# Kernel tuning notes

Measured on AMD Instinct MI355X. Metric: run time of the kernel, lower is better.

The kernel has to match this reference:

```python
import jax, jax.numpy as jnp
import numpy as np

TEMPERATURE = 8.0  # sqrt(dim_k=64)
NEG_INF = -1e30    # stand-in for -inf that stays finite-safe under softmax


def setup_inputs() -> dict:
    key = jax.random.key(0)
    kq, kk, kv, km = jax.random.split(key, 4)
    bsz, lq, lk, d = 64, 2048, 2048, 64
    q = jax.random.normal(kq, (bsz, lq, d), dtype=jnp.float32)
    k = jax.random.normal(kk, (bsz, lk, d), dtype=jnp.float32)
    v = jax.random.normal(kv, (bsz, lk, d), dtype=jnp.float32)
    mask = jax.random.normal(km, (bsz, lq, lk), dtype=jnp.float32)
    return {"q": q, "k": k, "v": v, "mask": mask}


def reference(q, k, v, mask):
    # attn = QK^T / temperature, additive graph mask, threshold -inf fill
    attn = jnp.einsum("bqd,bkd->bqk", q, k) / TEMPERATURE
    attn = attn + mask                       # graph_mask_type == 'add'
    attn = jnp.where(mask < 0, NEG_INF, attn)  # masked_fill(mask.lt(0), -inf)
    attn = jax.nn.softmax(attn, axis=2)
    # dropout p=0.0 -> identity
    output = jnp.einsum("bqk,bkd->bqd", attn, v)
    return (output, attn)
```

## Files before the change

kernel.cpp:

```cpp
#include <hip/hip_runtime.h>
#include <stdint.h>
#include <stddef.h>


typedef __attribute__((ext_vector_type(4))) float f32x4;
typedef __fp16 f16x2 __attribute__((ext_vector_type(2)));
typedef __fp16 f16x4 __attribute__((ext_vector_type(4)));
typedef __fp16 f16x8 __attribute__((ext_vector_type(8)));

static constexpr int BATCH = 64;
static constexpr int SEQ   = 2048;
static constexpr int HD    = 64;
static constexpr float NEGH = -60000.0f;


__global__ void cvt_f16_kernel(const float* __restrict__ in,
                               __fp16* __restrict__ out, int n4) {
  int i = blockIdx.x * blockDim.x + threadIdx.x;
  if (i >= n4) return;
  f32x4 v = *(const f32x4*)(in + (size_t)i * 4);
  f16x4 o;
  o[0] = (__fp16)v[0]; o[1] = (__fp16)v[1];
  o[2] = (__fp16)v[2]; o[3] = (__fp16)v[3];
  *(f16x4*)(out + (size_t)i * 4) = o;
}

__global__ __launch_bounds__(256, 2) void attn_kernel(
    const __fp16* __restrict__ qh,
    const __fp16* __restrict__ kh,
    const __fp16* __restrict__ vh,
    const float* __restrict__ mask,
    float* __restrict__ out,
    float* __restrict__ attn) {
  __shared__ __align__(16) char pool[4][11520];
  __shared__ float stat_m[4][16];
  __shared__ float stat_l[4][16];

  const int tid  = threadIdx.x;
  const int w    = tid >> 6;
  const int lane = tid & 63;
  const int l15  = lane & 15;
  const int g    = lane >> 4;
  const int g4   = g << 2;
  const int g8   = g << 3;
  const int krow = lane >> 3;
  const int kc16 = (lane & 7) * 16;

  const int bid = blockIdx.x;
  const int xcd = bid & 7;
  const int r   = bid >> 3;
  const int b   = xcd * 8 + (r >> 7);
  const int q0  = (r & 127) << 4;
  const int wk0 = w << 9;

  char* wb = pool[w];

  const __fp16* qptr = qh + ((size_t)(b * SEQ + q0 + l15)) * HD;
  const f16x8 qb0 = *(const f16x8*)(qptr + g8);
  const f16x8 qb1 = *(const f16x8*)(qptr + 32 + g8);

  const __fp16* kstrip = kh + ((size_t)(b * SEQ) + wk0) * HD;
  const __fp16* vstrip = vh + ((size_t)(b * SEQ) + wk0) * HD;
  const float*  mbase  = mask + ((size_t)(b * SEQ + q0)) * SEQ + wk0;
  float*        abase  = attn + ((size_t)(b * SEQ + q0)) * SEQ + wk0;

  f16x4 PH0,  PH1,  PH2,  PH3,  PH4,  PH5,  PH6,  PH7;
  f16x4 PH8,  PH9,  PH10, PH11, PH12, PH13, PH14, PH15;
  f16x4 PH16, PH17, PH18, PH19, PH20, PH21, PH22, PH23;
  f16x4 PH24, PH25, PH26, PH27, PH28, PH29, PH30, PH31;

  f16x8 K0A, K0B, K1A, K1B, K2A, K2B, K3A, K3B;
  f16x8 K4A, K4B, K5A, K5B, K6A, K6B, K7A, K7B;
  f32x4 MA0, MA1, MA2, MA3;
  f32x4 MB0, MB1, MB2, MB3;
  float m = -3.0e38f;

#define ISSUE_K(t, KA, KB)                                                   \
  KA = *(const f16x8*)(kstrip + (size_t)(t) * 1024 + lane * 8);              \
  KB = *(const f16x8*)(kstrip + (size_t)(t) * 1024 + 512 + lane * 8);

#define WRITE_K(s, KA, KB)                                                   \
  *(f16x8*)(wb + (s) * 2304 + krow * 144 + kc16) = KA;                       \
  *(f16x8*)(wb + (s) * 2304 + (8 + krow) * 144 + kc16) = KB;

#define ISSUE_M(c, M0, M1, M2, M3)                                           \
  M0 = __builtin_nontemporal_load((const f32x4*)(mbase + (size_t)(0 * 4 + g) * SEQ + (c) * 64 + l15 * 4)); \
  M1 = __builtin_nontemporal_load((const f32x4*)(mbase + (size_t)(1 * 4 + g) * SEQ + (c) * 64 + l15 * 4)); \
  M2 = __builtin_nontemporal_load((const f32x4*)(mbase + (size_t)(2 * 4 + g) * SEQ + (c) * 64 + l15 * 4)); \
  M3 = __builtin_nontemporal_load((const f32x4*)(mbase + (size_t)(3 * 4 + g) * SEQ + (c) * 64 + l15 * 4));

#define WRITE_M(M0, M1, M2, M3)                                              \
  *(f32x4*)(wb + 7168 + (0 * 4 + g) * 272 + l15 * 16) = M0;                  \
  *(f32x4*)(wb + 7168 + (1 * 4 + g) * 272 + l15 * 16) = M1;                  \
  *(f32x4*)(wb + 7168 + (2 * 4 + g) * 272 + l15 * 16) = M2;                  \
  *(f32x4*)(wb + 7168 + (3 * 4 + g) * 272 + l15 * 16) = M3;

#define ATILE(t, s, PH)                                                      \
  {                                                                          \
    const f16x8 fa = *(const f16x8*)(wb + (s) * 2304 + l15 * 144 + g * 16);  \
    const f16x8 fb = *(const f16x8*)(wb + (s) * 2304 + l15 * 144 + 64 + g * 16); \
    f32x4 acc = {0.f, 0.f, 0.f, 0.f};                                        \
    acc = __builtin_amdgcn_mfma_f32_16x16x32_f16(fa, qb0, acc, 0, 0, 0);     \
    acc = __builtin_amdgcn_mfma_f32_16x16x32_f16(fb, qb1, acc, 0, 0, 0);     \
    const f32x4 mv = *(const f32x4*)(wb + 7168 + l15 * 272 + ((t) & 3) * 64 + g * 16); \
    float s0 = (mv[0] < 0.f) ? NEGH : fmaf(acc[0], 0.125f, mv[0]);           \
    float s1 = (mv[1] < 0.f) ? NEGH : fmaf(acc[1], 0.125f, mv[1]);           \
    float s2 = (mv[2] < 0.f) ? NEGH : fmaf(acc[2], 0.125f, mv[2]);           \
    float s3 = (mv[3] < 0.f) ? NEGH : fmaf(acc[3], 0.125f, mv[3]);           \
    m = fmaxf(m, fmaxf(fmaxf(s0, s1), fmaxf(s2, s3)));                       \
    f16x2 lo_ = __builtin_amdgcn_cvt_pkrtz(s0, s1);                          \
    f16x2 hi_ = __builtin_amdgcn_cvt_pkrtz(s2, s3);                          \
    PH = (f16x4){lo_[0], lo_[1], hi_[0], hi_[1]};                            \
  }

#define AT(t, PH, KA, KB)                                                    \
  WRITE_K((t) & 1, KA, KB) ISSUE_K((t) + 8, KA, KB) ATILE(t, (t) & 1, PH)
#define ATL(t, PH, KA, KB)                                                   \
  WRITE_K((t) & 1, KA, KB) ATILE(t, (t) & 1, PH)

  ISSUE_M(0, MA0, MA1, MA2, MA3)
  ISSUE_K(0, K0A, K0B) ISSUE_K(1, K1A, K1B) ISSUE_K(2, K2A, K2B) ISSUE_K(3, K3A, K3B)
  ISSUE_M(1, MB0, MB1, MB2, MB3)
  ISSUE_K(4, K4A, K4B) ISSUE_K(5, K5A, K5B) ISSUE_K(6, K6A, K6B) ISSUE_K(7, K7A, K7B)

  WRITE_M(MA0, MA1, MA2, MA3) ISSUE_M(2, MA0, MA1, MA2, MA3)
  AT(0, PH0, K0A, K0B)  AT(1, PH1, K1A, K1B)  AT(2, PH2, K2A, K2B)  AT(3, PH3, K3A, K3B)
  WRITE_M(MB0, MB1, MB2, MB3) ISSUE_M(3, MB0, MB1, MB2, MB3)
  AT(4, PH4, K4A, K4B)  AT(5, PH5, K5A, K5B)  AT(6, PH6, K6A, K6B)  AT(7, PH7, K7A, K7B)
  WRITE_M(MA0, MA1, MA2, MA3) ISSUE_M(4, MA0, MA1, MA2, MA3)
  AT(8, PH8, K0A, K0B)  AT(9, PH9, K1A, K1B)  AT(10, PH10, K2A, K2B) AT(11, PH11, K3A, K3B)
  WRITE_M(MB0, MB1, MB2, MB3) ISSUE_M(5, MB0, MB1, MB2, MB3)
  AT(12, PH12, K4A, K4B) AT(13, PH13, K5A, K5B) AT(14, PH14, K6A, K6B) AT(15, PH15, K7A, K7B)
  WRITE_M(MA0, MA1, MA2, MA3) ISSUE_M(6, MA0, MA1, MA2, MA3)
  AT(16, PH16, K0A, K0B) AT(17, PH17, K1A, K1B) AT(18, PH18, K2A, K2B) AT(19, PH19, K3A, K3B)
  WRITE_M(MB0, MB1, MB2, MB3) ISSUE_M(7, MB0, MB1, MB2, MB3)
  AT(20, PH20, K4A, K4B) AT(21, PH21, K5A, K5B) AT(22, PH22, K6A, K6B) AT(23, PH23, K7A, K7B)
  WRITE_M(MA0, MA1, MA2, MA3)
  ATL(24, PH24, K0A, K0B) ATL(25, PH25, K1A, K1B) ATL(26, PH26, K2A, K2B) ATL(27, PH27, K3A, K3B)
  WRITE_M(MB0, MB1, MB2, MB3)
  ATL(28, PH28, K4A, K4B) ATL(29, PH29, K5A, K5B) ATL(30, PH30, K6A, K6B) ATL(31, PH31, K7A, K7B)

#undef AT
#undef ATL
#undef ATILE
#undef ISSUE_K
#undef WRITE_K
#undef ISSUE_M
#undef WRITE_M

  m = fmaxf(m, __shfl_xor(m, 16));
  m = fmaxf(m, __shfl_xor(m, 32));

  float lw = 0.f;
#define A2_STEP(PH)                                                          \
  {                                                                          \
    float e0 = __expf((float)PH[0] - m);                                     \
    float e1 = __expf((float)PH[1] - m);                                     \
    float e2 = __expf((float)PH[2] - m);                                     \
    float e3 = __expf((float)PH[3] - m);                                     \
    lw += (e0 + e1) + (e2 + e3);                                             \
    f16x2 lo_ = __builtin_amdgcn_cvt_pkrtz(e0, e1);                          \
    f16x2 hi_ = __builtin_amdgcn_cvt_pkrtz(e2, e3);                          \
    PH = (f16x4){lo_[0], lo_[1], hi_[0], hi_[1]};                            \
  }
  A2_STEP(PH0)  A2_STEP(PH1)  A2_STEP(PH2)  A2_STEP(PH3)
  A2_STEP(PH4)  A2_STEP(PH5)  A2_STEP(PH6)  A2_STEP(PH7)
  A2_STEP(PH8)  A2_STEP(PH9)  A2_STEP(PH10) A2_STEP(PH11)
  A2_STEP(PH12) A2_STEP(PH13) A2_STEP(PH14) A2_STEP(PH15)
  A2_STEP(PH16) A2_STEP(PH17) A2_STEP(PH18) A2_STEP(PH19)
  A2_STEP(PH20) A2_STEP(PH21) A2_STEP(PH22) A2_STEP(PH23)
  A2_STEP(PH24) A2_STEP(PH25) A2_STEP(PH26) A2_STEP(PH27)
  A2_STEP(PH28) A2_STEP(PH29) A2_STEP(PH30) A2_STEP(PH31)
#undef A2_STEP

  lw += __shfl_xor(lw, 16);
  lw += __shfl_xor(lw, 32);

  if (lane < 16) { stat_m[w][lane] = m; stat_l[w][lane] = lw; }
  __syncthreads();

  float mg = -3.0e38f;
#pragma unroll
  for (int ww = 0; ww < 4; ++ww) mg = fmaxf(mg, stat_m[ww][l15]);
  float lg = 0.f;
#pragma unroll
  for (int ww = 0; ww < 4; ++ww) lg += stat_l[ww][l15] * __expf(stat_m[ww][l15] - mg);
  const float scale = __expf(m - mg) / lg;
  const __fp16 hs = (__fp16)scale;
  const f16x4 sc4 = {hs, hs, hs, hs};

  f32x4 oacc0 = {0.f, 0.f, 0.f, 0.f};
  f32x4 oacc1 = {0.f, 0.f, 0.f, 0.f};
  f32x4 oacc2 = {0.f, 0.f, 0.f, 0.f};
  f32x4 oacc3 = {0.f, 0.f, 0.f, 0.f};

  f16x8 V0A, V0B, V1A, V1B, V2A, V2B, V3A, V3B;

#define ISSUE_V(t, VA, VB)                                                   \
  VA = *(const f16x8*)(vstrip + (size_t)(t) * 1024 + lane * 8);              \
  VB = *(const f16x8*)(vstrip + (size_t)(t) * 1024 + 512 + lane * 8);

#define WRITE_VT(VA, VB)                                                     \
  {                                                                          \
    char* p_ = wb + 4608 + ((lane & 7) * 8) * 40 + krow * 2;                 \
    *(__fp16*)(p_ + 0 * 40) = VA[0]; *(__fp16*)(p_ + 1 * 40) = VA[1];        \
    *(__fp16*)(p_ + 2 * 40) = VA[2]; *(__fp16*)(p_ + 3 * 40) = VA[3];        \
    *(__fp16*)(p_ + 4 * 40) = VA[4]; *(__fp16*)(p_ + 5 * 40) = VA[5];        \
    *(__fp16*)(p_ + 6 * 40) = VA[6]; *(__fp16*)(p_ + 7 * 40) = VA[7];        \
    char* q_ = p_ + 16;                                                      \
    *(__fp16*)(q_ + 0 * 40) = VB[0]; *(__fp16*)(q_ + 1 * 40) = VB[1];        \
    *(__fp16*)(q_ + 2 * 40) = VB[2]; *(__fp16*)(q_ + 3 * 40) = VB[3];        \
    *(__fp16*)(q_ + 4 * 40) = VB[4]; *(__fp16*)(q_ + 5 * 40) = VB[5];        \
    *(__fp16*)(q_ + 6 * 40) = VB[6]; *(__fp16*)(q_ + 7 * 40) = VB[7];        \
  }

#define BTILE(t, PH)                                                         \
  {                                                                          \
    const f16x4 pf = PH * sc4;                                               \
    f32x4 st;                                                                \
    st[0] = (float)pf[0]; st[1] = (float)pf[1];                              \
    st[2] = (float)pf[2]; st[3] = (float)pf[3];                              \
    *(f32x4*)(wb + 7168 + l15 * 272 + ((t) & 3) * 64 + g * 16) = st;         \
    const char* vf_ = wb + 4608 + l15 * 40 + g * 8;                          \
    const f16x4 Vr0_ = *(const f16x4*)(vf_ + 0 * 640);                       \
    const f16x4 Vr1_ = *(const f16x4*)(vf_ + 1 * 640);                       \
    const f16x4 Vr2_ = *(const f16x4*)(vf_ + 2 * 640);                       \
    const f16x4 Vr3_ = *(const f16x4*)(vf_ + 3 * 640);                       \
    oacc0 = __builtin_amdgcn_mfma_f32_16x16x16f16(Vr0_, pf, oacc0, 0, 0, 0); \
    oacc1 = __builtin_amdgcn_mfma_f32_16x16x16f16(Vr1_, pf, oacc1, 0, 0, 0); \
    oacc2 = __builtin_amdgcn_mfma_f32_16x16x16f16(Vr2_, pf, oacc2, 0, 0, 0); \
    oacc3 = __builtin_amdgcn_mfma_f32_16x16x16f16(Vr3_, pf, oacc3, 0, 0, 0); \
  }

#define STORE_A(c)                                                           \
  __builtin_nontemporal_store(                                               \
      *(const f32x4*)(wb + 7168 + (0 * 4 + g) * 272 + l15 * 16),             \
      (f32x4*)(abase + (size_t)(0 * 4 + g) * SEQ + (c) * 64 + l15 * 4));     \
  __builtin_nontemporal_store(                                               \
      *(const f32x4*)(wb + 7168 + (1 * 4 + g) * 272 + l15 * 16),             \
      (f32x4*)(abase + (size_t)(1 * 4 + g) * SEQ + (c) * 64 + l15 * 4));     \
  __builtin_nontemporal_store(                                               \
      *(const f32x4*)(wb + 7168 + (2 * 4 + g) * 272 + l15 * 16),             \
      (f32x4*)(abase + (size_t)(2 * 4 + g) * SEQ + (c) * 64 + l15 * 4));     \
  __builtin_nontemporal_store(                                               \
      *(const f32x4*)(wb + 7168 + (3 * 4 + g) * 272 + l15 * 16),             \
      (f32x4*)(abase + (size_t)(3 * 4 + g) * SEQ + (c) * 64 + l15 * 4));

#define BSTEP(t, PH, VA, VB)   BTILE(t, PH) WRITE_VT(VA, VB) ISSUE_V((t) + 5, VA, VB)
#define BSTEPN(t, PH, VA, VB)  BTILE(t, PH) WRITE_VT(VA, VB)
#define BSTEPL(t, PH)          BTILE(t, PH)

  ISSUE_V(0, V0A, V0B) ISSUE_V(1, V1A, V1B) ISSUE_V(2, V2A, V2B) ISSUE_V(3, V3A, V3B)
  WRITE_VT(V0A, V0B)
  ISSUE_V(4, V0A, V0B)

  BSTEP(0, PH0, V1A, V1B)   BSTEP(1, PH1, V2A, V2B)   BSTEP(2, PH2, V3A, V3B)
  BSTEP(3, PH3, V0A, V0B)   STORE_A(0)
  BSTEP(4, PH4, V1A, V1B)   BSTEP(5, PH5, V2A, V2B)   BSTEP(6, PH6, V3A, V3B)
  BSTEP(7, PH7, V0A, V0B)   STORE_A(1)
  BSTEP(8, PH8, V1A, V1B)   BSTEP(9, PH9, V2A, V2B)   BSTEP(10, PH10, V3A, V3B)
  BSTEP(11, PH11, V0A, V0B) STORE_A(2)
  BSTEP(12, PH12, V1A, V1B) BSTEP(13, PH13, V2A, V2B) BSTEP(14, PH14, V3A, V3B)
  BSTEP(15, PH15, V0A, V0B) STORE_A(3)
  BSTEP(16, PH16, V1A, V1B) BSTEP(17, PH17, V2A, V2B) BSTEP(18, PH18, V3A, V3B)
  BSTEP(19, PH19, V0A, V0B) STORE_A(4)
  BSTEP(20, PH20, V1A, V1B) BSTEP(21, PH21, V2A, V2B) BSTEP(22, PH22, V3A, V3B)
  BSTEP(23, PH23, V0A, V0B) STORE_A(5)
  BSTEP(24, PH24, V1A, V1B) BSTEP(25, PH25, V2A, V2B) BSTEP(26, PH26, V3A, V3B)
  BSTEPN(27, PH27, V0A, V0B) STORE_A(6)
  BSTEPN(28, PH28, V1A, V1B) BSTEPN(29, PH29, V2A, V2B) BSTEPN(30, PH30, V3A, V3B)
  BSTEPL(31, PH31)           STORE_A(7)

#undef BSTEP
#undef BSTEPN
#undef BSTEPL
#undef BTILE
#undef WRITE_VT
#undef ISSUE_V
#undef STORE_A

  float* sred_w = (float*)pool[w];
#pragma unroll
  for (int rr = 0; rr < 4; ++rr) {
    sred_w[(0 * 16 + g4 + rr) * 17 + l15] = oacc0[rr];
    sred_w[(1 * 16 + g4 + rr) * 17 + l15] = oacc1[rr];
    sred_w[(2 * 16 + g4 + rr) * 17 + l15] = oacc2[rr];
    sred_w[(3 * 16 + g4 + rr) * 17 + l15] = oacc3[rr];
  }
  __syncthreads();

#pragma unroll
  for (int ii = 0; ii < 4; ++ii) {
    const int i = tid + ii * 256;
    const int q = i >> 6;
    const int d = i & 63;
    const int o = d * 17 + q;
    float s = ((const float*)pool[0])[o] + ((const float*)pool[1])[o] +
              ((const float*)pool[2])[o] + ((const float*)pool[3])[o];
    out[((size_t)(b * SEQ + q0 + q)) * HD + d] = s;
  }
}

extern "C" void kernel_launch(void* const* d_in, const int* in_sizes, int n_in,
                              void* d_out, int out_size, void* d_ws, size_t ws_size,
                              hipStream_t stream) {
  const float* q    = (const float*)d_in[0];
  const float* k    = (const float*)d_in[1];
  const float* v    = (const float*)d_in[2];
  const float* mask = (const float*)d_in[3];

  float* out  = (float*)d_out;
  float* attn = out + (size_t)BATCH * SEQ * HD;

  const size_t nqk = (size_t)BATCH * SEQ * HD;
  __fp16* qh = (__fp16*)d_ws;
  __fp16* kh = qh + nqk;
  __fp16* vhf = kh + nqk;

  const int n4 = (int)(nqk / 4);
  cvt_f16_kernel<<<dim3((n4 + 255) / 256), dim3(256), 0, stream>>>(q, qh, n4);
  cvt_f16_kernel<<<dim3((n4 + 255) / 256), dim3(256), 0, stream>>>(k, kh, n4);
  cvt_f16_kernel<<<dim3((n4 + 255) / 256), dim3(256), 0, stream>>>(v, vhf, n4);
  attn_kernel<<<dim3(BATCH * (SEQ / 16)), dim3(256), 0, stream>>>(qh, kh, vhf, mask, out, attn);
}
```

Before: 571.4 us.

## Pre-swizzle K and V into MFMA fragment layout, drop LDS staging

Replaces the generic f16 conversion kernels with kernels that write K and V directly in per-lane MFMA fragment order (V transposed), so the attention kernel loads operands straight into registers without LDS writes and reads. Q conversion is fused into the attention kernel, which removes one launch and one pass over Q. LDS per wave shrinks, possibly helping occupancy. In exchange the V prep kernel does an LDS transpose, and global loads are now smaller and more scattered.

Result: faster. 540.0 us (-5.5%).

```diff
diff --git a/kernel.cpp b/kernel.cpp
--- a/kernel.cpp
+++ b/kernel.cpp
@@ -13,26 +13,76 @@
 static constexpr int HD    = 64;
 static constexpr float NEGH = -60000.0f;
 
-
-__global__ void cvt_f16_kernel(const float* __restrict__ in,
-                               __fp16* __restrict__ out, int n4) {
-  int i = blockIdx.x * blockDim.x + threadIdx.x;
-  if (i >= n4) return;
-  f32x4 v = *(const f32x4*)(in + (size_t)i * 4);
-  f16x4 o;
-  o[0] = (__fp16)v[0]; o[1] = (__fp16)v[1];
-  o[2] = (__fp16)v[2]; o[3] = (__fp16)v[3];
-  *(f16x4*)(out + (size_t)i * 4) = o;
+__global__ void kfrag_kernel(const float* __restrict__ k, __fp16* __restrict__ kf) {
+  const int b    = blockIdx.x >> 5;
+  const int ch   = blockIdx.x & 31;
+  const int tid  = threadIdx.x;
+  const int tl   = tid >> 6;
+  const int lane = tid & 63;
+  const int l15  = lane & 15;
+  const int g    = lane >> 4;
+  const int kt   = ch * 4 + tl;
+  const float* src = k + ((size_t)(b * SEQ + kt * 16 + l15)) * HD + g * 8;
+  char* dst = (char*)kf + ((size_t)(b * 128 + kt)) * 2048 + l15 * 64 + g * 16;
+#pragma unroll
+  for (int half = 0; half < 2; ++half) {
+    f32x4 a = *(const f32x4*)(src + half * 32);
+    f32x4 c = *(const f32x4*)(src + half * 32 + 4);
+    f16x2 p0 = __builtin_amdgcn_cvt_pkrtz(a[0], a[1]);
+    f16x2 p1 = __builtin_amdgcn_cvt_pkrtz(a[2], a[3]);
+    f16x2 p2 = __builtin_amdgcn_cvt_pkrtz(c[0], c[1]);
+    f16x2 p3 = __builtin_amdgcn_cvt_pkrtz(c[2], c[3]);
+    f16x8 o;
+    o[0] = p0[0]; o[1] = p0[1]; o[2] = p1[0]; o[3] = p1[1];
+    o[4] = p2[0]; o[5] = p2[1]; o[6] = p3[0]; o[7] = p3[1];
+    *(f16x8*)(dst + half * 1024) = o;
+  }
 }
 
+__global__ void vfrag_kernel(const float* __restrict__ v, __fp16* __restrict__ vf) {
+  __shared__ float tile[64][68];
+  const int b   = blockIdx.x >> 5;
+  const int ch  = blockIdx.x & 31;
+  const int tid = threadIdx.x;
+  const int kk  = tid >> 4;
+  const int d4  = (tid & 15) << 2;
+  const int k0  = ch * 64;
+#pragma unroll
+  for (int i = 0; i < 4; ++i) {
+    f32x4 val = *(const f32x4*)(v + ((size_t)(b * SEQ + k0 + kk + 16 * i)) * HD + d4);
+    tile[kk + 16 * i][d4 + 0] = val[0];
+    tile[kk + 16 * i][d4 + 1] = val[1];
+    tile[kk + 16 * i][d4 + 2] = val[2];
+    tile[kk + 16 * i][d4 + 3] = val[3];
+  }
+  __syncthreads();
+  const int tl  = tid >> 6;
+  const int db  = (tid >> 4) & 3;
+  const int l15 = tid & 15;
+  f16x8 o0, o1;
+#pragma unroll
+  for (int g = 0; g < 2; ++g)
+#pragma unroll
+    for (int j = 0; j < 4; ++j)
+      o0[g * 4 + j] = (__fp16)tile[tl * 16 + g * 4 + j][db * 16 + l15];
+#pragma unroll
+  for (int g = 0; g < 2; ++g)
+#pragma unroll
+    for (int j = 0; j < 4; ++j)
+      o1[g * 4 + j] = (__fp16)tile[tl * 16 + (g + 2) * 4 + j][db * 16 + l15];
+  char* dst = (char*)vf + ((size_t)(b * 128 + ch * 4 + tl)) * 2048 + db * 512 + l15 * 32;
+  *(f16x8*)(dst)      = o0;
+  *(f16x8*)(dst + 16) = o1;
+}
+
 __global__ __launch_bounds__(256, 2) void attn_kernel(
-    const __fp16* __restrict__ qh,
-    const __fp16* __restrict__ kh,
-    const __fp16* __restrict__ vh,
+    const float* __restrict__ q,
+    const __fp16* __restrict__ kf,
+    const __fp16* __restrict__ vf,
     const float* __restrict__ mask,
     float* __restrict__ out,
     float* __restrict__ attn) {
-  __shared__ __align__(16) char pool[4][11520];
+  __shared__ __align__(16) char pool[4][4352];
   __shared__ float stat_m[4][16];
   __shared__ float stat_l[4][16];
 
@@ -42,9 +92,6 @@
   const int l15  = lane & 15;
   const int g    = lane >> 4;
   const int g4   = g << 2;
-  const int g8   = g << 3;
-  const int krow = lane >> 3;
-  const int kc16 = (lane & 7) * 16;
 
   const int bid = blockIdx.x;
   const int xcd = bid & 7;
@@ -54,15 +101,34 @@
   const int wk0 = w << 9;
 
   char* wb = pool[w];
-
-  const __fp16* qptr = qh + ((size_t)(b * SEQ + q0 + l15)) * HD;
-  const f16x8 qb0 = *(const f16x8*)(qptr + g8);
-  const f16x8 qb1 = *(const f16x8*)(qptr + 32 + g8);
-
-  const __fp16* kstrip = kh + ((size_t)(b * SEQ) + wk0) * HD;
-  const __fp16* vstrip = vh + ((size_t)(b * SEQ) + wk0) * HD;
-  const float*  mbase  = mask + ((size_t)(b * SEQ + q0)) * SEQ + wk0;
-  float*        abase  = attn + ((size_t)(b * SEQ + q0)) * SEQ + wk0;
+  const int koff = l15 * 64 + g * 16;
+  const int voff = l15 * 32 + g * 8;
+
+  const char* kfb = (const char*)kf + ((size_t)(b * 128) + w * 32) * 2048;
+  const char* vfb = (const char*)vf + ((size_t)(b * 128) + w * 32) * 2048;
+  const float* mbase = mask + ((size_t)(b * SEQ + q0)) * SEQ + wk0;
+  float*       abase = attn + ((size_t)(b * SEQ + q0)) * SEQ + wk0;
+
+  f16x8 qb0, qb1;
+  {
+    const float* qsrc = q + ((size_t)(b * SEQ + q0 + l15)) * HD + g * 8;
+    f32x4 a0 = *(const f32x4*)(qsrc);
+    f32x4 a1 = *(const f32x4*)(qsrc + 4);
+    f32x4 c0 = *(const f32x4*)(qsrc + 32);
+    f32x4 c1 = *(const f32x4*)(qsrc + 36);
+    f16x2 p0 = __builtin_amdgcn_cvt_pkrtz(a0[0], a0[1]);
+    f16x2 p1 = __builtin_amdgcn_cvt_pkrtz(a0[2], a0[3]);
+    f16x2 p2 = __builtin_amdgcn_cvt_pkrtz(a1[0], a1[1]);
+    f16x2 p3 = __builtin_amdgcn_cvt_pkrtz(a1[2], a1[3]);
+    qb0[0] = p0[0]; qb0[1] = p0[1]; qb0[2] = p1[0]; qb0[3] = p1[1];
+    qb0[4] = p2[0]; qb0[5] = p2[1]; qb0[6] = p3[0]; qb0[7] = p3[1];
+    p0 = __builtin_amdgcn_cvt_pkrtz(c0[0], c0[1]);
+    p1 = __builtin_amdgcn_cvt_pkrtz(c0[2], c0[3]);
+    p2 = __builtin_amdgcn_cvt_pkrtz(c1[0], c1[1]);
+    p3 = __builtin_amdgcn_cvt_pkrtz(c1[2], c1[3]);
+    qb1[0] = p0[0]; qb1[1] = p0[1]; qb1[2] = p1[0]; qb1[3] = p1[1];
+    qb1[4] = p2[0]; qb1[5] = p2[1]; qb1[6] = p3[0]; qb1[7] = p3[1];
+  }
 
   f16x4 PH0,  PH1,  PH2,  PH3,  PH4,  PH5,  PH6,  PH7;
   f16x4 PH8,  PH9,  PH10, PH11, PH12, PH13, PH14, PH15;
@@ -76,12 +142,8 @@
   float m = -3.0e38f;
 
 #define ISSUE_K(t, KA, KB)                                                   \
-  KA = *(const f16x8*)(kstrip + (size_t)(t) * 1024 + lane * 8);              \
-  KB = *(const f16x8*)(kstrip + (size_t)(t) * 1024 + 512 + lane * 8);
-
-#define WRITE_K(s, KA, KB)                                                   \
-  *(f16x8*)(wb + (s) * 2304 + krow * 144 + kc16) = KA;                       \
-  *(f16x8*)(wb + (s) * 2304 + (8 + krow) * 144 + kc16) = KB;
+  KA = *(const f16x8*)(kfb + (size_t)(t) * 2048 + koff);                     \
+  KB = *(const f16x8*)(kfb + (size_t)(t) * 2048 + 1024 + koff);
 
 #define ISSUE_M(c, M0, M1, M2, M3)                                           \
   M0 = __builtin_nontemporal_load((const f32x4*)(mbase + (size_t)(0 * 4 + g) * SEQ + (c) * 64 + l15 * 4)); \
@@ -90,19 +152,17 @@
   M3 = __builtin_nontemporal_load((const f32x4*)(mbase + (size_t)(3 * 4 + g) * SEQ + (c) * 64 + l15 * 4));
 
 #define WRITE_M(M0, M1, M2, M3)                                              \
-  *(f32x4*)(wb + 7168 + (0 * 4 + g) * 272 + l15 * 16) = M0;                  \
-  *(f32x4*)(wb + 7168 + (1 * 4 + g) * 272 + l15 * 16) = M1;                  \
-  *(f32x4*)(wb + 7168 + (2 * 4 + g) * 272 + l15 * 16) = M2;                  \
-  *(f32x4*)(wb + 7168 + (3 * 4 + g) * 272 + l15 * 16) = M3;
-
-#define ATILE(t, s, PH)                                                      \
+  *(f32x4*)(wb + (0 * 4 + g) * 272 + l15 * 16) = M0;                         \
+  *(f32x4*)(wb + (1 * 4 + g) * 272 + l15 * 16) = M1;                         \
+  *(f32x4*)(wb + (2 * 4 + g) * 272 + l15 * 16) = M2;                         \
+  *(f32x4*)(wb + (3 * 4 + g) * 272 + l15 * 16) = M3;
+
+#define ATILE(t, PH, KA, KB)                                                 \
   {                                                                          \
-    const f16x8 fa = *(const f16x8*)(wb + (s) * 2304 + l15 * 144 + g * 16);  \
-    const f16x8 fb = *(const f16x8*)(wb + (s) * 2304 + l15 * 144 + 64 + g * 16); \
     f32x4 acc = {0.f, 0.f, 0.f, 0.f};                                        \
-    acc = __builtin_amdgcn_mfma_f32_16x16x32_f16(fa, qb0, acc, 0, 0, 0);     \
-    acc = __builtin_amdgcn_mfma_f32_16x16x32_f16(fb, qb1, acc, 0, 0, 0);     \
-    const f32x4 mv = *(const f32x4*)(wb + 7168 + l15 * 272 + ((t) & 3) * 64 + g * 16); \
+    acc = __builtin_amdgcn_mfma_f32_16x16x32_f16(KA, qb0, acc, 0, 0, 0);     \
+    acc = __builtin_amdgcn_mfma_f32_16x16x32_f16(KB, qb1, acc, 0, 0, 0);     \
+    const f32x4 mv = *(const f32x4*)(wb + l15 * 272 + ((t) & 3) * 64 + g * 16); \
     float s0 = (mv[0] < 0.f) ? NEGH : fmaf(acc[0], 0.125f, mv[0]);           \
     float s1 = (mv[1] < 0.f) ? NEGH : fmaf(acc[1], 0.125f, mv[1]);           \
     float s2 = (mv[2] < 0.f) ? NEGH : fmaf(acc[2], 0.125f, mv[2]);           \
@@ -113,10 +173,8 @@
     PH = (f16x4){lo_[0], lo_[1], hi_[0], hi_[1]};                            \
   }
 
-#define AT(t, PH, KA, KB)                                                    \
-  WRITE_K((t) & 1, KA, KB) ISSUE_K((t) + 8, KA, KB) ATILE(t, (t) & 1, PH)
-#define ATL(t, PH, KA, KB)                                                   \
-  WRITE_K((t) & 1, KA, KB) ATILE(t, (t) & 1, PH)
+#define AT(t, PH, KA, KB)  ATILE(t, PH, KA, KB) ISSUE_K((t) + 8, KA, KB)
+#define ATL(t, PH, KA, KB) ATILE(t, PH, KA, KB)
 
   ISSUE_M(0, MA0, MA1, MA2, MA3)
   ISSUE_K(0, K0A, K0B) ISSUE_K(1, K1A, K1B) ISSUE_K(2, K2A, K2B) ISSUE_K(3, K3A, K3B)
@@ -144,7 +202,6 @@
 #undef ATL
 #undef ATILE
 #undef ISSUE_K
-#undef WRITE_K
 #undef ISSUE_M
 #undef WRITE_M
 
@@ -194,88 +251,68 @@
   f32x4 oacc2 = {0.f, 0.f, 0.f, 0.f};
   f32x4 oacc3 = {0.f, 0.f, 0.f, 0.f};
 
-  f16x8 V0A, V0B, V1A, V1B, V2A, V2B, V3A, V3B;
-
-#define ISSUE_V(t, VA, VB)                                                   \
-  VA = *(const f16x8*)(vstrip + (size_t)(t) * 1024 + lane * 8);              \
-  VB = *(const f16x8*)(vstrip + (size_t)(t) * 1024 + 512 + lane * 8);
-
-#define WRITE_VT(VA, VB)                                                     \
-  {                                                                          \
-    char* p_ = wb + 4608 + ((lane & 7) * 8) * 40 + krow * 2;                 \
-    *(__fp16*)(p_ + 0 * 40) = VA[0]; *(__fp16*)(p_ + 1 * 40) = VA[1];        \
-    *(__fp16*)(p_ + 2 * 40) = VA[2]; *(__fp16*)(p_ + 3 * 40) = VA[3];        \
-    *(__fp16*)(p_ + 4 * 40) = VA[4]; *(__fp16*)(p_ + 5 * 40) = VA[5];        \
-    *(__fp16*)(p_ + 6 * 40) = VA[6]; *(__fp16*)(p_ + 7 * 40) = VA[7];        \
-    char* q_ = p_ + 16;                                                      \
-    *(__fp16*)(q_ + 0 * 40) = VB[0]; *(__fp16*)(q_ + 1 * 40) = VB[1];        \
-    *(__fp16*)(q_ + 2 * 40) = VB[2]; *(__fp16*)(q_ + 3 * 40) = VB[3];        \
-    *(__fp16*)(q_ + 4 * 40) = VB[4]; *(__fp16*)(q_ + 5 * 40) = VB[5];        \
-    *(__fp16*)(q_ + 6 * 40) = VB[6]; *(__fp16*)(q_ + 7 * 40) = VB[7];        \
-  }
-
-#define BTILE(t, PH)                                                         \
+  f16x4 V0a, V0b, V0c, V0d, V1a, V1b, V1c, V1d;
+  f16x4 V2a, V2b, V2c, V2d, V3a, V3b, V3c, V3d;
+
+#define ISSUE_V(t, Va, Vb, Vc, Vd)                                           \
+  Va = *(const f16x4*)(vfb + (size_t)(t) * 2048 + 0 * 512 + voff);           \
+  Vb = *(const f16x4*)(vfb + (size_t)(t) * 2048 + 1 * 512 + voff);           \
+  Vc = *(const f16x4*)(vfb + (size_t)(t) * 2048 + 2 * 512 + voff);           \
+  Vd = *(const f16x4*)(vfb + (size_t)(t) * 2048 + 3 * 512 + voff);
+
+#define BTILE(t, PH, Va, Vb, Vc, Vd)                                         \
   {                                                                          \
     const f16x4 pf = PH * sc4;                                               \
     f32x4 st;                                                                \
     st[0] = (float)pf[0]; st[1] = (float)pf[1];                              \
     st[2] = (float)pf[2]; st[3] = (float)pf[3];                              \
-    *(f32x4*)(wb + 7168 + l15 * 272 + ((t) & 3) * 64 + g * 16) = st;         \
-    const char* vf_ = wb + 4608 + l15 * 40 + g * 8;                          \
-    const f16x4 Vr0_ = *(const f16x4*)(vf_ + 0 * 640);                       \
-    const f16x4 Vr1_ = *(const f16x4*)(vf_ + 1 * 640);                       \
-    const f16x4 Vr2_ = *(const f16x4*)(vf_ + 2 * 640);                       \
-    const f16x4 Vr3_ = *(const f16x4*)(vf_ + 3 * 640);                       \
-    oacc0 = __builtin_amdgcn_mfma_f32_16x16x16f16(Vr0_, pf, oacc0, 0, 0, 0); \
-    oacc1 = __builtin_amdgcn_mfma_f32_16x16x16f16(Vr1_, pf, oacc1, 0, 0, 0); \
-    oacc2 = __builtin_amdgcn_mfma_f32_16x16x16f16(Vr2_, pf, oacc2, 0, 0, 0); \
-    oacc3 = __builtin_amdgcn_mfma_f32_16x16x16f16(Vr3_, pf, oacc3, 0, 0, 0); \
+    *(f32x4*)(wb + l15 * 272 + ((t) & 3) * 64 + g * 16) = st;                \
+    oacc0 = __builtin_amdgcn_mfma_f32_16x16x16f16(Va, pf, oacc0, 0, 0, 0);   \
+    oacc1 = __builtin_amdgcn_mfma_f32_16x16x16f16(Vb, pf, oacc1, 0, 0, 0);   \
+    oacc2 = __builtin_amdgcn_mfma_f32_16x16x16f16(Vc, pf, oacc2, 0, 0, 0);   \
+    oacc3 = __builtin_amdgcn_mfma_f32_16x16x16f16(Vd, pf, oacc3, 0, 0, 0);   \
   }
 
 #define STORE_A(c)                                                           \
   __builtin_nontemporal_store(                                               \
-      *(const f32x4*)(wb + 7168 + (0 * 4 + g) * 272 + l15 * 16),             \
+      *(const f32x4*)(wb + (0 * 4 + g) * 272 + l15 * 16),                    \
       (f32x4*)(abase + (size_t)(0 * 4 + g) * SEQ + (c) * 64 + l15 * 4));     \
   __builtin_nontemporal_store(                                               \
-      *(const f32x4*)(wb + 7168 + (1 * 4 + g) * 272 + l15 * 16),             \
+      *(const f32x4*)(wb + (1 * 4 + g) * 272 + l15 * 16),                    \
       (f32x4*)(abase + (size_t)(1 * 4 + g) * SEQ + (c) * 64 + l15 * 4));     \
   __builtin_nontemporal_store(                                               \
-      *(const f32x4*)(wb + 7168 + (2 * 4 + g) * 272 + l15 * 16),             \
+      *(const f32x4*)(wb + (2 * 4 + g) * 272 + l15 * 16),                    \
       (f32x4*)(abase + (size_t)(2 * 4 + g) * SEQ + (c) * 64 + l15 * 4));     \
   __builtin_nontemporal_store(                                               \
-      *(const f32x4*)(wb + 7168 + (3 * 4 + g) * 272 + l15 * 16),             \
+      *(const f32x4*)(wb + (3 * 4 + g) * 272 + l15 * 16),                    \
       (f32x4*)(abase + (size_t)(3 * 4 + g) * SEQ + (c) * 64 + l15 * 4));
 
-#define BSTEP(t, PH, VA, VB)   BTILE(t, PH) WRITE_VT(VA, VB) ISSUE_V((t) + 5, VA, VB)
-#define BSTEPN(t, PH, VA, VB)  BTILE(t, PH) WRITE_VT(VA, VB)
-#define BSTEPL(t, PH)          BTILE(t, PH)
-
-  ISSUE_V(0, V0A, V0B) ISSUE_V(1, V1A, V1B) ISSUE_V(2, V2A, V2B) ISSUE_V(3, V3A, V3B)
-  WRITE_VT(V0A, V0B)
-  ISSUE_V(4, V0A, V0B)
-
-  BSTEP(0, PH0, V1A, V1B)   BSTEP(1, PH1, V2A, V2B)   BSTEP(2, PH2, V3A, V3B)
-  BSTEP(3, PH3, V0A, V0B)   STORE_A(0)
-  BSTEP(4, PH4, V1A, V1B)   BSTEP(5, PH5, V2A, V2B)   BSTEP(6, PH6, V3A, V3B)
-  BSTEP(7, PH7, V0A, V0B)   STORE_A(1)
-  BSTEP(8, PH8, V1A, V1B)   BSTEP(9, PH9, V2A, V2B)   BSTEP(10, PH10, V3A, V3B)
-  BSTEP(11, PH11, V0A, V0B) STORE_A(2)
-  BSTEP(12, PH12, V1A, V1B) BSTEP(13, PH13, V2A, V2B) BSTEP(14, PH14, V3A, V3B)
-  BSTEP(15, PH15, V0A, V0B) STORE_A(3)
-  BSTEP(16, PH16, V1A, V1B) BSTEP(17, PH17, V2A, V2B) BSTEP(18, PH18, V3A, V3B)
-  BSTEP(19, PH19, V0A, V0B) STORE_A(4)
-  BSTEP(20, PH20, V1A, V1B) BSTEP(21, PH21, V2A, V2B) BSTEP(22, PH22, V3A, V3B)
-  BSTEP(23, PH23, V0A, V0B) STORE_A(5)
-  BSTEP(24, PH24, V1A, V1B) BSTEP(25, PH25, V2A, V2B) BSTEP(26, PH26, V3A, V3B)
-  BSTEPN(27, PH27, V0A, V0B) STORE_A(6)
-  BSTEPN(28, PH28, V1A, V1B) BSTEPN(29, PH29, V2A, V2B) BSTEPN(30, PH30, V3A, V3B)
-  BSTEPL(31, PH31)           STORE_A(7)
-
-#undef BSTEP
-#undef BSTEPN
-#undef BSTEPL
+#define BS(t, PH, Va, Vb, Vc, Vd)  BTILE(t, PH, Va, Vb, Vc, Vd) ISSUE_V((t) + 4, Va, Vb, Vc, Vd)
+#define BSL(t, PH, Va, Vb, Vc, Vd) BTILE(t, PH, Va, Vb, Vc, Vd)
+
+  ISSUE_V(0, V0a, V0b, V0c, V0d) ISSUE_V(1, V1a, V1b, V1c, V1d)
+  ISSUE_V(2, V2a, V2b, V2c, V2d) ISSUE_V(3, V3a, V3b, V3c, V3d)
+
+  BS(0, PH0, V0a, V0b, V0c, V0d)   BS(1, PH1, V1a, V1b, V1c, V1d)
+  BS(2, PH2, V2a, V2b, V2c, V2d)   BS(3, PH3, V3a, V3b, V3c, V3d)   STORE_A(0)
+  BS(4, PH4, V0a, V0b, V0c, V0d)   BS(5, PH5, V1a, V1b, V1c, V1d)
+  BS(6, PH6, V2a, V2b, V2c, V2d)   BS(7, PH7, V3a, V3b, V3c, V3d)   STORE_A(1)
+  BS(8, PH8, V0a, V0b, V0c, V0d)   BS(9, PH9, V1a, V1b, V1c, V1d)
+  BS(10, PH10, V2a, V2b, V2c, V2d) BS(11, PH11, V3a, V3b, V3c, V3d) STORE_A(2)
+  BS(12, PH12, V0a, V0b, V0c, V0d) BS(13, PH13, V1a, V1b, V1c, V1d)
+  BS(14, PH14, V2a, V2b, V2c, V2d) BS(15, PH15, V3a, V3b, V3c, V3d) STORE_A(3)
+  BS(16, PH16, V0a, V0b, V0c, V0d) BS(17, PH17, V1a, V1b, V1c, V1d)
+  BS(18, PH18, V2a, V2b, V2c, V2d) BS(19, PH19, V3a, V3b, V3c, V3d) STORE_A(4)
+  BS(20, PH20, V0a, V0b, V0c, V0d) BS(21, PH21, V1a, V1b, V1c, V1d)
+  BS(22, PH22, V2a, V2b, V2c, V2d) BS(23, PH23, V3a, V3b, V3c, V3d) STORE_A(5)
+  BS(24, PH24, V0a, V0b, V0c, V0d) BS(25, PH25, V1a, V1b, V1c, V1d)
+  BS(26, PH26, V2a, V2b, V2c, V2d) BS(27, PH27, V3a, V3b, V3c, V3d) STORE_A(6)
+  BSL(28, PH28, V0a, V0b, V0c, V0d) BSL(29, PH29, V1a, V1b, V1c, V1d)
+  BSL(30, PH30, V2a, V2b, V2c, V2d) BSL(31, PH31, V3a, V3b, V3c, V3d) STORE_A(7)
+
+#undef BS
+#undef BSL
 #undef BTILE
-#undef WRITE_VT
 #undef ISSUE_V
 #undef STORE_A
 
@@ -292,12 +329,12 @@
 #pragma unroll
   for (int ii = 0; ii < 4; ++ii) {
     const int i = tid + ii * 256;
-    const int q = i >> 6;
+    const int qq = i >> 6;
     const int d = i & 63;
-    const int o = d * 17 + q;
+    const int o = d * 17 + qq;
     float s = ((const float*)pool[0])[o] + ((const float*)pool[1])[o] +
               ((const float*)pool[2])[o] + ((const float*)pool[3])[o];
-    out[((size_t)(b * SEQ + q0 + q)) * HD + d] = s;
+    out[((size_t)(b * SEQ + q0 + qq)) * HD + d] = s;
   }
 }
 
@@ -313,13 +350,10 @@
   float* attn = out + (size_t)BATCH * SEQ * HD;
 
   const size_t nqk = (size_t)BATCH * SEQ * HD;
-  __fp16* qh = (__fp16*)d_ws;
-  __fp16* kh = qh + nqk;
-  __fp16* vhf = kh + nqk;
-
-  const int n4 = (int)(nqk / 4);
-  cvt_f16_kernel<<<dim3((n4 + 255) / 256), dim3(256), 0, stream>>>(q, qh, n4);
-  cvt_f16_kernel<<<dim3((n4 + 255) / 256), dim3(256), 0, stream>>>(k, kh, n4);
-  cvt_f16_kernel<<<dim3((n4 + 255) / 256), dim3(256), 0, stream>>>(v, vhf, n4);
-  attn_kernel<<<dim3(BATCH * (SEQ / 16)), dim3(256), 0, stream>>>(qh, kh, vhf, mask, out, attn);
+  __fp16* kfrag = (__fp16*)d_ws;
+  __fp16* vfrag = kfrag + nqk;
+
+  kfrag_kernel<<<dim3(BATCH * 32), dim3(256), 0, stream>>>(k, kfrag);
+  vfrag_kernel<<<dim3(BATCH * 32), dim3(256), 0, stream>>>(v, vfrag);
+  attn_kernel<<<dim3(BATCH * (SEQ / 16)), dim3(256), 0, stream>>>(q, kfrag, vfrag, mask, out, attn);
 }
```
